# Optimization experiments

Hardware: AMD Instinct MI355X
Metric: run time of the kernel (lower is better)

The kernel has to match this reference:

```python
import jax, jax.numpy as jnp
import numpy as np

B, N, C = 4, 2048, 1024
HEADS, DHEAD = 16, 64
EPS = 1e-7
SCALE = DHEAD ** (-0.5)


def setup_inputs() -> dict:
    key = jax.random.key(0)
    k1, k2, k3, k4 = jax.random.split(key, 4)
    inner = HEADS * DHEAD
    return {
        "x": jax.random.normal(k1, (B, N, C), dtype=jnp.float32),
        "gamma": jnp.ones((1, 1, C), dtype=jnp.float32),
        "Wq": jax.random.normal(k2, (inner, C), dtype=jnp.float32) * np.sqrt(1.0 / C),
        "Wkv": jax.random.normal(k3, (2 * DHEAD, C), dtype=jnp.float32) * np.sqrt(1.0 / C),
        "Wo": jax.random.normal(k4, (C, inner), dtype=jnp.float32) * np.sqrt(1.0 / inner) * 1e-5,
        "ls_scale": jnp.full((C,), 1e-4, dtype=jnp.float32),
    }


def reference(x, gamma, Wq, Wkv, Wo, ls_scale):
    # BiasFreeLayerNorm: divide by unbiased std (no mean subtraction), scale by gamma
    std = jnp.std(x, axis=-1, ddof=1, keepdims=True)
    xn = (x / (std + EPS)) * gamma
    # q from normalized x, k/v from the ORIGINAL x (kv_input = x before norm)
    q = xn @ Wq.T                       # [B, N, H*D]
    kv = x @ Wkv.T                      # [B, N, 2*D]
    k, v = kv[..., :DHEAD], kv[..., DHEAD:]  # shared single kv head (MQA)
    q = q.reshape(B, N, HEADS, DHEAD).transpose(0, 2, 1, 3) * SCALE  # [B, H, N, D]
    sim = jnp.einsum('bhid,bjd->bhij', q, k)
    attn = jax.nn.softmax(sim, axis=-1)
    out = jnp.einsum('bhij,bjd->bhid', attn, v)       # [B, H, N, D]
    out = out.transpose(0, 2, 1, 3).reshape(B, N, HEADS * DHEAD)
    out = out @ Wo.T
    return ls_scale * out
```

## Files before the change

### kernel.cpp

```cpp
#include <hip/hip_runtime.h>
#include <hip/hip_bf16.h>
#include <stdint.h>

typedef __attribute__((ext_vector_type(8))) short short8;
typedef __attribute__((ext_vector_type(4))) short short4v;
typedef __attribute__((ext_vector_type(4))) float f32x4;
typedef __attribute__((ext_vector_type(4))) unsigned short us4;

#define B_ 4
#define N_ 2048
#define C_ 1024
#define H_ 16
#define D_ 64

__device__ __forceinline__ unsigned short f2bf(float f) {
  union { float f; unsigned u; } v; v.f = f;
  unsigned u = v.u;
  u += 0x7fffu + ((u >> 16) & 1u);
  return (unsigned short)(u >> 16);
}

__device__ __forceinline__ unsigned short bfc(float f) {
  union { __hip_bfloat16 h; unsigned short u; } v;
  v.h = __float2bfloat16(f);
  return v.u;
}

__device__ __forceinline__ void glds16(const unsigned short* g, const unsigned short* l) {
  __builtin_amdgcn_global_load_lds(
      (const __attribute__((address_space(1))) void*)(uintptr_t)g,
      (__attribute__((address_space(3))) void*)(uintptr_t)l, 16, 0, 0);
}

__device__ __forceinline__ f32x4 mfma16(short8 a, short8 b, f32x4 c) {
  return __builtin_amdgcn_mfma_f32_16x16x32_bf16(a, b, c, 0, 0, 0);
}

#if __has_builtin(__builtin_amdgcn_mfma_f32_16x16x16bf16_1k)
__device__ __forceinline__ f32x4 mfma16b(short4v a, short4v b, f32x4 c) {
  return __builtin_amdgcn_mfma_f32_16x16x16bf16_1k(a, b, c, 0, 0, 0);
}
#else
__device__ __forceinline__ f32x4 mfma16b(short4v a, short4v b, f32x4 c) {
  asm volatile("v_mfma_f32_16x16x16_bf16 %0, %1, %2, %0\n\ts_nop 7\n\ts_nop 7"
               : "+v"(c) : "v"(a), "v"(b));
  return c;
}
#endif

__global__ __launch_bounds__(256) void prep_cast_k(const float* __restrict__ x,
                                                   const float* __restrict__ gamma,
                                                   unsigned short* __restrict__ xn,
                                                   unsigned short* __restrict__ xb,
                                                   const float* __restrict__ wq,
                                                   const float* __restrict__ wkv,
                                                   const float* __restrict__ wo,
                                                   unsigned short* __restrict__ dq,
                                                   unsigned short* __restrict__ dkv,
                                                   unsigned short* __restrict__ dwo) {
  const int t = threadIdx.x;
  if (blockIdx.x >= 8192) {
    const int i = (blockIdx.x - 8192) * 256 + t;
    const float* s;
    unsigned short* d;
    int j;
    if (i < 262144) { s = wq; d = dq; j = i; }
    else if (i < 294912) { s = wkv; d = dkv; j = i - 262144; }
    else { s = wo; d = dwo; j = i - 294912; }
    const float4 v = ((const float4*)s)[j];
    us4 o; o.x = f2bf(v.x); o.y = f2bf(v.y); o.z = f2bf(v.z); o.w = f2bf(v.w);
    ((us4*)d)[j] = o;
    return;
  }
  const int row = blockIdx.x;
  const float4 v = ((const float4*)(x + (size_t)row * C_))[t];
  float s1 = v.x + v.y + v.z + v.w;
  float s2 = v.x * v.x + v.y * v.y + v.z * v.z + v.w * v.w;
#pragma unroll
  for (int off = 32; off > 0; off >>= 1) {
    s1 += __shfl_down(s1, off);
    s2 += __shfl_down(s2, off);
  }
  __shared__ float r1[4], r2[4];
  if ((t & 63) == 0) { r1[t >> 6] = s1; r2[t >> 6] = s2; }
  __syncthreads();
  s1 = r1[0] + r1[1] + r1[2] + r1[3];
  s2 = r2[0] + r2[1] + r2[2] + r2[3];
  const float var = (s2 - s1 * s1 * (1.0f / C_)) * (1.0f / (C_ - 1));
  const float rstd = 1.0f / (sqrtf(var) + 1e-7f);
  const float4 gv = ((const float4*)gamma)[t];
  us4 a, b;
  a.x = f2bf(v.x); a.y = f2bf(v.y); a.z = f2bf(v.z); a.w = f2bf(v.w);
  b.x = f2bf(v.x * rstd * gv.x); b.y = f2bf(v.y * rstd * gv.y);
  b.z = f2bf(v.z * rstd * gv.z); b.w = f2bf(v.w * rstd * gv.w);
  ((us4*)(xb + (size_t)row * C_))[t] = a;
  ((us4*)(xn + (size_t)row * C_))[t] = b;
}

__global__ __launch_bounds__(256) void vtrans_k(const unsigned short* __restrict__ kvb,
                                                unsigned short* __restrict__ vtb) {
  __shared__ unsigned short T[64][68];
  const int t = threadIdx.x, nt = blockIdx.x;
  const int r = t >> 2, c4 = t & 3;
  const unsigned short* src = kvb + (size_t)(nt * 64 + r) * 128 + 64 + c4 * 16;
  *(short8*)&T[r][c4 * 16] = *(const short8*)src;
  *(short8*)&T[r][c4 * 16 + 8] = *(const short8*)(src + 8);
  __syncthreads();
  const int d = t >> 2, nq = t & 3;
  const int b = nt >> 5, nn0 = (nt & 31) * 64 + nq * 16;
  unsigned short* dst = vtb + ((size_t)b * 64 + d) * 2048 + nn0;
  short8 o0, o1;
#pragma unroll
  for (int j = 0; j < 8; ++j) {
    o0[j] = (short)T[nq * 16 + j][d];
    o1[j] = (short)T[nq * 16 + 8 + j][d];
  }
  if ((d >> 3) & 1) {
    o0 = __builtin_shufflevector(o0, o0, 4, 5, 6, 7, 0, 1, 2, 3);
    o1 = __builtin_shufflevector(o1, o1, 4, 5, 6, 7, 0, 1, 2, 3);
  }
  *(short8*)dst = o0;
  *(short8*)(dst + 8) = o1;
}

__global__ __launch_bounds__(256, 2) void qkv_gemm(const unsigned short* __restrict__ xn,
                                                   const unsigned short* __restrict__ xb,
                                                   const unsigned short* __restrict__ wq,
                                                   const unsigned short* __restrict__ wkv,
                                                   unsigned short* __restrict__ qo,
                                                   unsigned short* __restrict__ kvo) {
  const bool iskv = (blockIdx.x == 8);
  const unsigned short* A = iskv ? xb : xn;
  const unsigned short* Bw = iskv ? wkv : wq;
  unsigned short* Cc = iskv ? kvo : qo;
  const int N = iskv ? 128 : 1024;
  const int n0 = iskv ? 0 : blockIdx.x * 128;
  const float uscale = iskv ? 1.0f : 0.18033688011112042f;
  const int K = 1024, m0 = blockIdx.y * 128;

  __shared__ unsigned short At[128 * 32];
  __shared__ unsigned short Bt[128 * 32];
  const int t = threadIdx.x;
  const int w = t >> 6, l = t & 63;
  const int ql = l & 15, g = l >> 4;
  const int wr = (w >> 1) * 64, wc = (w & 1) * 64;

  const int pr0 = t >> 2, pb0 = t & 3;
  const int lb0 = pb0 ^ ((pr0 >> 1) & 3);
  const int pr1 = 64 + (t >> 2);
  const int lb1 = pb0 ^ ((pr1 >> 1) & 3);
  const unsigned short* Ab = A + (size_t)m0 * K;
  const unsigned short* Bb = Bw + (size_t)n0 * K;

  f32x4 acc[4][4];
#pragma unroll
  for (int i = 0; i < 4; ++i)
#pragma unroll
    for (int j = 0; j < 4; ++j) acc[i][j] = f32x4{0.f, 0.f, 0.f, 0.f};

  for (int k0 = 0; k0 < K; k0 += 32) {
    glds16(Ab + (size_t)pr0 * K + k0 + lb0 * 8, &At[w * 512]);
    glds16(Ab + (size_t)pr1 * K + k0 + lb1 * 8, &At[2048 + w * 512]);
    glds16(Bb + (size_t)pr0 * K + k0 + lb0 * 8, &Bt[w * 512]);
    glds16(Bb + (size_t)pr1 * K + k0 + lb1 * 8, &Bt[2048 + w * 512]);
    __syncthreads();
    short8 af[4], bfr[4];
#pragma unroll
    for (int i = 0; i < 4; ++i) {
      const int row = wr + i * 16 + ql;
      af[i] = *(const short8*)&At[row * 32 + ((g ^ ((row >> 1) & 3)) * 8)];
    }
#pragma unroll
    for (int i = 0; i < 4; ++i) {
      const int row = wc + i * 16 + ql;
      bfr[i] = *(const short8*)&Bt[row * 32 + ((g ^ ((row >> 1) & 3)) * 8)];
    }
#pragma unroll
    for (int mi = 0; mi < 4; ++mi)
#pragma unroll
      for (int ni = 0; ni < 4; ++ni)
        acc[mi][ni] = mfma16(af[mi], bfr[ni], acc[mi][ni]);
    __syncthreads();
  }

#pragma unroll
  for (int mi = 0; mi < 4; ++mi)
#pragma unroll
    for (int ni = 0; ni < 4; ++ni) {
      const int col = n0 + wc + ni * 16 + ql;
#pragma unroll
      for (int r = 0; r < 4; ++r) {
        const int row = m0 + wr + mi * 16 + g * 4 + r;
        Cc[(size_t)row * N + col] = f2bf(acc[mi][ni][r] * uscale);
      }
    }
}

__global__ __launch_bounds__(256, 2) void gemm_o(const unsigned short* __restrict__ A,
                                                 const unsigned short* __restrict__ Bw,
                                                 float* __restrict__ Cout,
                                                 const float* __restrict__ colscale,
                                                 int M, int N, int K) {
  __shared__ unsigned short At[128 * 32];
  __shared__ unsigned short Bt[128 * 32];
  const int t = threadIdx.x;
  const int w = t >> 6, l = t & 63;
  const int ql = l & 15, g = l >> 4;
  const int wr = (w >> 1) * 64, wc = (w & 1) * 64;
  const int m0 = blockIdx.y * 128, n0 = blockIdx.x * 128;

  const int pr0 = t >> 2, pb0 = t & 3;
  const int lb0 = pb0 ^ ((pr0 >> 1) & 3);
  const int pr1 = 64 + (t >> 2);
  const int lb1 = pb0 ^ ((pr1 >> 1) & 3);
  const unsigned short* Ab = A + (size_t)m0 * K;
  const unsigned short* Bb = Bw + (size_t)n0 * K;

  f32x4 acc[4][4];
#pragma unroll
  for (int i = 0; i < 4; ++i)
#pragma unroll
    for (int j = 0; j < 4; ++j) acc[i][j] = f32x4{0.f, 0.f, 0.f, 0.f};

  for (int k0 = 0; k0 < K; k0 += 32) {
    glds16(Ab + (size_t)pr0 * K + k0 + lb0 * 8, &At[w * 512]);
    glds16(Ab + (size_t)pr1 * K + k0 + lb1 * 8, &At[2048 + w * 512]);
    glds16(Bb + (size_t)pr0 * K + k0 + lb0 * 8, &Bt[w * 512]);
    glds16(Bb + (size_t)pr1 * K + k0 + lb1 * 8, &Bt[2048 + w * 512]);
    __syncthreads();
    short8 af[4], bfr[4];
#pragma unroll
    for (int i = 0; i < 4; ++i) {
      const int row = wr + i * 16 + ql;
      af[i] = *(const short8*)&At[row * 32 + ((g ^ ((row >> 1) & 3)) * 8)];
    }
#pragma unroll
    for (int i = 0; i < 4; ++i) {
      const int row = wc + i * 16 + ql;
      bfr[i] = *(const short8*)&Bt[row * 32 + ((g ^ ((row >> 1) & 3)) * 8)];
    }
#pragma unroll
    for (int mi = 0; mi < 4; ++mi)
#pragma unroll
      for (int ni = 0; ni < 4; ++ni)
        acc[mi][ni] = mfma16(af[mi], bfr[ni], acc[mi][ni]);
    __syncthreads();
  }

#pragma unroll
  for (int mi = 0; mi < 4; ++mi)
#pragma unroll
    for (int ni = 0; ni < 4; ++ni) {
      const int col = n0 + wc + ni * 16 + ql;
      const float cs = colscale[col];
#pragma unroll
      for (int r = 0; r < 4; ++r) {
        const int row = m0 + wr + mi * 16 + g * 4 + r;
        Cout[(size_t)row * N + col] = acc[mi][ni][r] * cs;
      }
    }
}

__global__ __launch_bounds__(256, 3) void attn_k(const unsigned short* __restrict__ qb,
                                                 const unsigned short* __restrict__ kvb,
                                                 const unsigned short* __restrict__ vtb,
                                                 unsigned short* __restrict__ ao) {
  __shared__ unsigned short Kt[2][64 * 64];
  __shared__ unsigned short Vt[2][64 * 64];

  const int idx = blockIdx.x;
  const int qc = idx & 15, hd = (idx >> 4) & 15, b = idx >> 8;
  const int t = threadIdx.x, w = t >> 6, l = t & 63;
  const int ql = l & 15, g = l >> 4;
  const int q0 = qc * 128 + w * 32;

  const unsigned short* qbase = qb + (size_t)(b * N_ + q0) * C_ + hd * D_;
  short8 Qf[2][2];
#pragma unroll
  for (int qs = 0; qs < 2; ++qs)
#pragma unroll
    for (int h = 0; h < 2; ++h)
      Qf[qs][h] = *(const short8*)(qbase + (size_t)(16 * qs + ql) * C_ + 32 * h + 8 * g);

  const unsigned short* kvrow = kvb + (size_t)(b * N_) * 128;
  const unsigned short* vtrow = vtb + (size_t)b * 64 * 2048;
  const int sr = l >> 3;
  const int blk = ((l & 7) ^ sr) << 3;
  const int row0 = 16 * w + sr;
  const int row1 = row0 + 8;
  const int sw = ql & 7;
  const int hb = (ql >> 3) & 1;

  auto stage = [&](int bi, int kt) {
    glds16(kvrow + (size_t)(kt * 64 + row0) * 128 + blk, &Kt[bi][(2 * w) * 512]);
    glds16(kvrow + (size_t)(kt * 64 + row1) * 128 + blk, &Kt[bi][(2 * w + 1) * 512]);
    glds16(vtrow + (size_t)row0 * 2048 + kt * 64 + blk, &Vt[bi][(2 * w) * 512]);
    glds16(vtrow + (size_t)row1 * 2048 + kt * 64 + blk, &Vt[bi][(2 * w + 1) * 512]);
  };

  f32x4 o[2][4];
#pragma unroll
  for (int qs = 0; qs < 2; ++qs)
#pragma unroll
    for (int dt = 0; dt < 4; ++dt) o[qs][dt] = f32x4{0.f, 0.f, 0.f, 0.f};
  float m[2] = {-1e30f, -1e30f}, lsum[2] = {0.f, 0.f};

  auto tilec = [&](int bi) {
    short8 Kf[4][2];
#pragma unroll
    for (int c = 0; c < 4; ++c) {
      const int roff = (16 * c + ql) * 64;
      Kf[c][0] = *(const short8*)&Kt[bi][roff + ((g ^ sw) << 3)];
      Kf[c][1] = *(const short8*)&Kt[bi][roff + (((g + 4) ^ sw) << 3)];
    }
    short4v pa[2][4];
#pragma unroll
    for (int qs = 0; qs < 2; ++qs) {
      f32x4 s[4];
#pragma unroll
      for (int c = 0; c < 4; ++c) {
        f32x4 acc = {0.f, 0.f, 0.f, 0.f};
        acc = mfma16(Kf[c][0], Qf[qs][0], acc);
        acc = mfma16(Kf[c][1], Qf[qs][1], acc);
        s[c] = acc;
      }
      float t0 = fmaxf(s[0][0], fmaxf(s[0][1], s[0][2]));
      float t1 = fmaxf(s[0][3], fmaxf(s[1][0], s[1][1]));
      float t2 = fmaxf(s[1][2], fmaxf(s[1][3], s[2][0]));
      float t3 = fmaxf(s[2][1], fmaxf(s[2][2], s[2][3]));
      float t4 = fmaxf(s[3][0], fmaxf(s[3][1], s[3][2]));
      float tm = fmaxf(s[3][3], fmaxf(t0, t1));
      tm = fmaxf(tm, fmaxf(t2, fmaxf(t3, t4)));
      if (!__all(tm <= m[qs] + 8.0f)) {
        float tmr = fmaxf(tm, __shfl_xor(tm, 16));
        tmr = fmaxf(tmr, __shfl_xor(tmr, 32));
        const float mn = fmaxf(m[qs], tmr);
        const float corr = __builtin_amdgcn_exp2f(m[qs] - mn);
        lsum[qs] *= corr;
#pragma unroll
        for (int dt = 0; dt < 4; ++dt) o[qs][dt] *= corr;
        m[qs] = mn;
      }
      float ps = 0.f;
#pragma unroll
      for (int c = 0; c < 4; ++c) {
        const float p0 = __builtin_amdgcn_exp2f(s[c][0] - m[qs]);
        const float p1 = __builtin_amdgcn_exp2f(s[c][1] - m[qs]);
        const float p2 = __builtin_amdgcn_exp2f(s[c][2] - m[qs]);
        const float p3 = __builtin_amdgcn_exp2f(s[c][3] - m[qs]);
        ps += (p0 + p1) + (p2 + p3);
        short4v pv;
        pv[0] = (short)bfc(p0); pv[1] = (short)bfc(p1);
        pv[2] = (short)bfc(p2); pv[3] = (short)bfc(p3);
        pa[qs][c] = pv;
      }
      lsum[qs] += ps;
    }

    __builtin_amdgcn_s_setprio(1);
#pragma unroll
    for (int dt = 0; dt < 4; ++dt) {
      const int vro = (16 * dt + ql) * 64 + 4 * ((g & 1) ^ hb);
      short4v Vf[4];
#pragma unroll
      for (int c = 0; c < 4; ++c)
        Vf[c] = *(const short4v*)&Vt[bi][vro + (((2 * c + (g >> 1)) ^ sw) << 3)];
#pragma unroll
      for (int qs = 0; qs < 2; ++qs)
#pragma unroll
        for (int c = 0; c < 4; ++c)
          o[qs][dt] = mfma16b(Vf[c], pa[qs][c], o[qs][dt]);
    }
    __builtin_amdgcn_s_setprio(0);
  };

  stage(0, 0);
  for (int kt = 0; kt < 32; kt += 2) {
    __syncthreads();
    stage(1, kt + 1);
    tilec(0);
    __syncthreads();
    if (kt + 2 < 32) stage(0, kt + 2);
    tilec(1);
  }

#pragma unroll
  for (int qs = 0; qs < 2; ++qs) {
    lsum[qs] += __shfl_xor(lsum[qs], 16);
    lsum[qs] += __shfl_xor(lsum[qs], 32);
  }

#pragma unroll
  for (int qs = 0; qs < 2; ++qs) {
    const float inv = 1.0f / lsum[qs];
    unsigned short* orow = ao + (size_t)(b * N_ + q0 + 16 * qs + ql) * C_ + hd * D_;
#pragma unroll
    for (int dt = 0; dt < 4; ++dt) {
      us4 st;
      st.x = bfc(o[qs][dt][0] * inv);
      st.y = bfc(o[qs][dt][1] * inv);
      st.z = bfc(o[qs][dt][2] * inv);
      st.w = bfc(o[qs][dt][3] * inv);
      *(us4*)(orow + dt * 16 + 4 * g) = st;
    }
  }
}

extern "C" void kernel_launch(void* const* d_in, const int* in_sizes, int n_in,
                              void* d_out, int out_size, void* d_ws, size_t ws_size,
                              hipStream_t stream) {
  const float* x = (const float*)d_in[0];
  const float* gamma = (const float*)d_in[1];
  const float* Wq = (const float*)d_in[2];
  const float* Wkv = (const float*)d_in[3];
  const float* Wo = (const float*)d_in[4];
  const float* ls = (const float*)d_in[5];
  float* out = (float*)d_out;

  unsigned short* ws = (unsigned short*)d_ws;
  const size_t R = (size_t)B_ * N_;
  unsigned short* xn = ws;
  unsigned short* xb = xn + R * C_;
  unsigned short* qbuf = xb + R * C_;
  unsigned short* kvb = qbuf + R * C_;
  unsigned short* aob = kvb + R * 128;
  unsigned short* wqb = aob + R * C_;
  unsigned short* wkvb = wqb + (size_t)C_ * C_;
  unsigned short* wob = wkvb + (size_t)128 * C_;
  unsigned short* vtb = wqb;

  prep_cast_k<<<(int)R + 2176, 256, 0, stream>>>(x, gamma, xn, xb,
                                                 Wq, Wkv, Wo, wqb, wkvb, wob);
  qkv_gemm<<<dim3(9, R / 128), 256, 0, stream>>>(xn, xb, wqb, wkvb, qbuf, kvb);
  vtrans_k<<<(int)(R / 64), 256, 0, stream>>>(kvb, vtb);
  attn_k<<<B_ * H_ * (N_ / 128), 256, 0, stream>>>(qbuf, kvb, vtb, aob);
  gemm_o<<<dim3(C_ / 128, R / 128), 256, 0, stream>>>(aob, wob, out, ls,
                                                      (int)R, C_, C_);
}
```

Measured before the change: 178.0 us.

## Fold layernorm scaling into Q epilogue and fuse V transpose into QKV GEMM

```diff
diff --git a/kernel.cpp b/kernel.cpp
--- a/kernel.cpp
+++ b/kernel.cpp
@@ -50,8 +50,8 @@
 
 __global__ __launch_bounds__(256) void prep_cast_k(const float* __restrict__ x,
                                                    const float* __restrict__ gamma,
-                                                   unsigned short* __restrict__ xn,
                                                    unsigned short* __restrict__ xb,
+                                                   float* __restrict__ rstd_v,
                                                    const float* __restrict__ wq,
                                                    const float* __restrict__ wkv,
                                                    const float* __restrict__ wo,
@@ -61,15 +61,23 @@
   const int t = threadIdx.x;
   if (blockIdx.x >= 8192) {
     const int i = (blockIdx.x - 8192) * 256 + t;
-    const float* s;
-    unsigned short* d;
-    int j;
-    if (i < 262144) { s = wq; d = dq; j = i; }
-    else if (i < 294912) { s = wkv; d = dkv; j = i - 262144; }
-    else { s = wo; d = dwo; j = i - 294912; }
-    const float4 v = ((const float4*)s)[j];
-    us4 o; o.x = f2bf(v.x); o.y = f2bf(v.y); o.z = f2bf(v.z); o.w = f2bf(v.w);
-    ((us4*)d)[j] = o;
+    if (i < 262144) {
+      const float4 v = ((const float4*)wq)[i];
+      const float4 gv = ((const float4*)gamma)[i & 255];
+      us4 o;
+      o.x = f2bf(v.x * gv.x); o.y = f2bf(v.y * gv.y);
+      o.z = f2bf(v.z * gv.z); o.w = f2bf(v.w * gv.w);
+      ((us4*)dq)[i] = o;
+    } else {
+      const float* s;
+      unsigned short* d;
+      int j;
+      if (i < 294912) { s = wkv; d = dkv; j = i - 262144; }
+      else { s = wo; d = dwo; j = i - 294912; }
+      const float4 v = ((const float4*)s)[j];
+      us4 o; o.x = f2bf(v.x); o.y = f2bf(v.y); o.z = f2bf(v.z); o.w = f2bf(v.w);
+      ((us4*)d)[j] = o;
+    }
     return;
   }
   const int row = blockIdx.x;
@@ -88,54 +96,22 @@
   s2 = r2[0] + r2[1] + r2[2] + r2[3];
   const float var = (s2 - s1 * s1 * (1.0f / C_)) * (1.0f / (C_ - 1));
   const float rstd = 1.0f / (sqrtf(var) + 1e-7f);
-  const float4 gv = ((const float4*)gamma)[t];
-  us4 a, b;
+  if (t == 0) rstd_v[row] = rstd;
+  us4 a;
   a.x = f2bf(v.x); a.y = f2bf(v.y); a.z = f2bf(v.z); a.w = f2bf(v.w);
-  b.x = f2bf(v.x * rstd * gv.x); b.y = f2bf(v.y * rstd * gv.y);
-  b.z = f2bf(v.z * rstd * gv.z); b.w = f2bf(v.w * rstd * gv.w);
   ((us4*)(xb + (size_t)row * C_))[t] = a;
-  ((us4*)(xn + (size_t)row * C_))[t] = b;
-}
-
-__global__ __launch_bounds__(256) void vtrans_k(const unsigned short* __restrict__ kvb,
-                                                unsigned short* __restrict__ vtb) {
-  __shared__ unsigned short T[64][68];
-  const int t = threadIdx.x, nt = blockIdx.x;
-  const int r = t >> 2, c4 = t & 3;
-  const unsigned short* src = kvb + (size_t)(nt * 64 + r) * 128 + 64 + c4 * 16;
-  *(short8*)&T[r][c4 * 16] = *(const short8*)src;
-  *(short8*)&T[r][c4 * 16 + 8] = *(const short8*)(src + 8);
-  __syncthreads();
-  const int d = t >> 2, nq = t & 3;
-  const int b = nt >> 5, nn0 = (nt & 31) * 64 + nq * 16;
-  unsigned short* dst = vtb + ((size_t)b * 64 + d) * 2048 + nn0;
-  short8 o0, o1;
-#pragma unroll
-  for (int j = 0; j < 8; ++j) {
-    o0[j] = (short)T[nq * 16 + j][d];
-    o1[j] = (short)T[nq * 16 + 8 + j][d];
-  }
-  if ((d >> 3) & 1) {
-    o0 = __builtin_shufflevector(o0, o0, 4, 5, 6, 7, 0, 1, 2, 3);
-    o1 = __builtin_shufflevector(o1, o1, 4, 5, 6, 7, 0, 1, 2, 3);
-  }
-  *(short8*)dst = o0;
-  *(short8*)(dst + 8) = o1;
-}
-
-__global__ __launch_bounds__(256, 2) void qkv_gemm(const unsigned short* __restrict__ xn,
-                                                   const unsigned short* __restrict__ xb,
+}
+
+__global__ __launch_bounds__(256, 2) void qkv_gemm(const unsigned short* __restrict__ xb,
                                                    const unsigned short* __restrict__ wq,
                                                    const unsigned short* __restrict__ wkv,
+                                                   const float* __restrict__ rstd_v,
                                                    unsigned short* __restrict__ qo,
-                                                   unsigned short* __restrict__ kvo) {
+                                                   unsigned short* __restrict__ kvo,
+                                                   unsigned short* __restrict__ vtb) {
   const bool iskv = (blockIdx.x == 8);
-  const unsigned short* A = iskv ? xb : xn;
   const unsigned short* Bw = iskv ? wkv : wq;
-  unsigned short* Cc = iskv ? kvo : qo;
-  const int N = iskv ? 128 : 1024;
   const int n0 = iskv ? 0 : blockIdx.x * 128;
-  const float uscale = iskv ? 1.0f : 0.18033688011112042f;
   const int K = 1024, m0 = blockIdx.y * 128;
 
   __shared__ unsigned short At[128 * 32];
@@ -149,7 +125,7 @@
   const int lb0 = pb0 ^ ((pr0 >> 1) & 3);
   const int pr1 = 64 + (t >> 2);
   const int lb1 = pb0 ^ ((pr1 >> 1) & 3);
-  const unsigned short* Ab = A + (size_t)m0 * K;
+  const unsigned short* Ab = xb + (size_t)m0 * K;
   const unsigned short* Bb = Bw + (size_t)n0 * K;
 
   f32x4 acc[4][4];
@@ -183,17 +159,55 @@
     __syncthreads();
   }
 
-#pragma unroll
-  for (int mi = 0; mi < 4; ++mi)
-#pragma unroll
-    for (int ni = 0; ni < 4; ++ni) {
-      const int col = n0 + wc + ni * 16 + ql;
-#pragma unroll
-      for (int r = 0; r < 4; ++r) {
-        const int row = m0 + wr + mi * 16 + g * 4 + r;
-        Cc[(size_t)row * N + col] = f2bf(acc[mi][ni][r] * uscale);
-      }
-    }
+  if (!iskv) {
+    float rs[4][4];
+#pragma unroll
+    for (int mi = 0; mi < 4; ++mi)
+#pragma unroll
+      for (int r = 0; r < 4; ++r)
+        rs[mi][r] = 0.18033688011112042f * rstd_v[m0 + wr + mi * 16 + g * 4 + r];
+#pragma unroll
+    for (int mi = 0; mi < 4; ++mi)
+#pragma unroll
+      for (int ni = 0; ni < 4; ++ni) {
+        const int col = n0 + wc + ni * 16 + ql;
+#pragma unroll
+        for (int r = 0; r < 4; ++r) {
+          const int row = m0 + wr + mi * 16 + g * 4 + r;
+          qo[(size_t)row * 1024 + col] = f2bf(acc[mi][ni][r] * rs[mi][r]);
+        }
+      }
+  } else if (wc == 0) {
+#pragma unroll
+    for (int mi = 0; mi < 4; ++mi)
+#pragma unroll
+      for (int ni = 0; ni < 4; ++ni) {
+        const int col = ni * 16 + ql;
+#pragma unroll
+        for (int r = 0; r < 4; ++r) {
+          const int row = m0 + wr + mi * 16 + g * 4 + r;
+          kvo[(size_t)row * 128 + col] = f2bf(acc[mi][ni][r]);
+        }
+      }
+  } else {
+    const int brow = m0 >> 11;
+    unsigned short* vb = vtb + (size_t)brow * 64 * 2048;
+#pragma unroll
+    for (int mi = 0; mi < 4; ++mi) {
+      const int nbase = (m0 & 2047) + wr + mi * 16 + g * 4;
+#pragma unroll
+      for (int ni = 0; ni < 4; ++ni) {
+        const int d = ni * 16 + ql;
+        const int nadj = nbase ^ (((d >> 3) & 1) ? 4 : 0);
+        us4 st;
+        st.x = f2bf(acc[mi][ni][0]);
+        st.y = f2bf(acc[mi][ni][1]);
+        st.z = f2bf(acc[mi][ni][2]);
+        st.w = f2bf(acc[mi][ni][3]);
+        *(us4*)&vb[(size_t)d * 2048 + nadj] = st;
+      }
+    }
+  }
 }
 
 __global__ __launch_bounds__(256, 2) void gemm_o(const unsigned short* __restrict__ A,
@@ -419,20 +433,20 @@
 
   unsigned short* ws = (unsigned short*)d_ws;
   const size_t R = (size_t)B_ * N_;
-  unsigned short* xn = ws;
-  unsigned short* xb = xn + R * C_;
+  unsigned short* xb = ws;
   unsigned short* qbuf = xb + R * C_;
   unsigned short* kvb = qbuf + R * C_;
   unsigned short* aob = kvb + R * 128;
   unsigned short* wqb = aob + R * C_;
   unsigned short* wkvb = wqb + (size_t)C_ * C_;
   unsigned short* wob = wkvb + (size_t)128 * C_;
-  unsigned short* vtb = wqb;
-
-  prep_cast_k<<<(int)R + 2176, 256, 0, stream>>>(x, gamma, xn, xb,
+  unsigned short* vtb = wob + (size_t)C_ * C_;
+  float* rstd = (float*)(vtb + (size_t)4 * 64 * 2048);
+
+  prep_cast_k<<<(int)R + 2176, 256, 0, stream>>>(x, gamma, xb, rstd,
                                                  Wq, Wkv, Wo, wqb, wkvb, wob);
-  qkv_gemm<<<dim3(9, R / 128), 256, 0, stream>>>(xn, xb, wqb, wkvb, qbuf, kvb);
-  vtrans_k<<<(int)(R / 64), 256, 0, stream>>>(kvb, vtb);
+  qkv_gemm<<<dim3(9, R / 128), 256, 0, stream>>>(xb, wqb, wkvb, rstd,
+                                                 qbuf, kvb, vtb);
   attn_k<<<B_ * H_ * (N_ / 128), 256, 0, stream>>>(qbuf, kvb, vtb, aob);
   gemm_o<<<dim3(C_ / 128, R / 128), 256, 0, stream>>>(aob, wob, out, ls,
                                                       (int)R, C_, C_);
```

New measurement: 173.1 us. 2.8% less time.
